# Performance work log

Hardware: AMD Instinct MI355X
Metric: run time of the kernel (lower is better)

Reference implementation:

```python
import jax, jax.numpy as jnp
import numpy as np

B = 32          # batch
NR = 1000       # n_reports
NP = 2000       # n_paths (candidate codes per lookup matrix)
NC = 3000       # n_codes (valid path / code entries)
NSNIP = 20000   # n_snippets
RV = 20000      # report word vocab
CV = 50000      # code word vocab
QL = 50         # report length (words)
S = 100         # num_snippet per code
L = 60          # len_snippet (words per snippet)
E = 300         # word embedding dim
DD = 100        # dim_dense
K = 5           # k_max_pool
NEG = 1.0e12


def setup_inputs() -> dict:
    key = jax.random.key(0)
    ks = jax.random.split(key, 16)
    f = jnp.float32
    sc = lambda n: 1.0 / float(np.sqrt(n))
    inp = {}
    inp["r_idx"] = jax.random.randint(ks[0], (B,), 0, NR)
    inp["c_idx"] = jax.random.randint(ks[1], (B,), 0, NP)
    # lookup tables stored as float (cast to int inside forward, as in torch)
    inp["matrix"] = jax.random.randint(ks[2], (NR, NP), 0, NC).astype(f)
    inp["report_table"] = jax.random.randint(ks[3], (NR, QL), 0, RV).astype(f)
    inp["report_word_emb"] = jax.random.normal(ks[4], (RV, E), dtype=f)
    inp["idf_table"] = jax.random.uniform(ks[5], (RV, 1), dtype=f, minval=0.5, maxval=6.0)
    inp["code_table"] = jax.random.randint(ks[6], (NC, S), 0, NSNIP).astype(f)
    inp["snippet_table"] = jax.random.randint(ks[7], (NSNIP, L), 0, CV).astype(f)
    inp["code_word_emb"] = jax.random.normal(ks[8], (CV, E), dtype=f)
    inp["snippet_len_table"] = jax.random.randint(ks[9], (NSNIP, 1), 1, L + 1).astype(f)
    inp["code_len_table"] = jax.random.randint(ks[10], (NP, 1), 1, S + 1).astype(f)
    # trainable relevance MLP + k-max fusion
    inp["W1"] = jax.random.uniform(ks[11], (E, DD), dtype=f, minval=-sc(E), maxval=sc(E))
    inp["b1"] = jnp.zeros((DD,), f)
    inp["W2"] = jax.random.uniform(ks[12], (DD, DD // 2), dtype=f, minval=-sc(DD), maxval=sc(DD))
    inp["b2"] = jnp.zeros((DD // 2,), f)
    inp["W3"] = jax.random.uniform(ks[13], (DD // 2, 1), dtype=f, minval=-sc(DD // 2), maxval=sc(DD // 2))
    inp["b3"] = jnp.zeros((1,), f)
    inp["Wk"] = jax.random.uniform(ks[14], (K, 1), dtype=f, minval=-sc(K), maxval=sc(K))
    inp["bk"] = jnp.zeros((1,), f)
    return inp


def _l2norm(x, axis):
    n = jnp.linalg.norm(x, ord=2, axis=axis, keepdims=True)
    y = x / n
    return jnp.where(jnp.isnan(y), 0.0, y)  # torch: NaN-fix after div


def reference(r_idx, c_idx, matrix, report_table, report_word_emb, idf_table,
              code_table, snippet_table, code_word_emb, snippet_len_table,
              code_len_table, W1, b1, W2, b2, W3, b3, Wk, bk):
    trans_c = matrix[r_idx, c_idx].astype(jnp.int32)            # (b,)
    r_vec = report_table[r_idx].astype(jnp.int32)               # (b,q)
    r_emb = report_word_emb[r_vec]                              # (b,q,e)
    c_snip = code_table[trans_c].astype(jnp.int32)              # (b,s)
    s_len = snippet_len_table[c_snip, 0].astype(jnp.int32)      # (b,s)
    c_words = snippet_table[c_snip].astype(jnp.int32)           # (b,s,l)
    c_emb = code_word_emb[c_words]                              # (b,s,l,e)
    s_mask = jnp.arange(L)[None, None, :] < s_len[:, :, None]   # (b,s,l)
    # masked dot attention: every report word attends within each snippet
    scores = jnp.einsum('bqe,bsle->bqsl', r_emb, c_emb)
    scores = scores - (~s_mask)[:, None, :, :].astype(scores.dtype) * NEG
    a = jax.nn.softmax(scores, axis=3)
    attn_v = jnp.einsum('bqsl,bsle->bqse', a, c_emb)            # (b,q,s,e)
    nc = _l2norm(attn_v, 3)                                     # (b,q,s,e)
    nr = _l2norm(r_emb, 2)                                      # (b,q,e)
    rc = nr[:, :, None, :] * nc                                 # (b,q,s,e)
    h = jnp.tanh(rc @ W1 + b1)
    h = jnp.tanh(h @ W2 + b2)
    rel = jnp.tanh(h @ W3 + b3)[..., 0]                         # (b,q,s)
    c_len = code_len_table[c_idx, 0].astype(jnp.int32)          # (b,)
    c_mask = (jnp.arange(S)[None, :] < c_len[:, None]).astype(rel.dtype)
    rel = rel * c_mask[:, None, :]
    topk = jax.lax.top_k(rel, K)[0]                             # (b,q,k)
    r_c = (topk @ Wk + bk)[..., 0]                              # (b,q)
    r_idf = idf_table[r_vec, 0]                                 # (b,q)
    r_idf = jnp.where(r_idf == 0.0, -NEG, r_idf)
    r_idf = jax.nn.softmax(r_idf, axis=1)
    return jnp.sum(r_c * r_idf, axis=1)                         # (b,)
```

## Files before the change

kernel.cpp:

```cpp
#include <hip/hip_runtime.h>
#include <math.h>

typedef __attribute__((ext_vector_type(8))) _Float16 half8;
typedef __attribute__((ext_vector_type(4))) _Float16 half4v;
typedef __attribute__((ext_vector_type(4))) float f32x4;

constexpr int cB = 32, cNP = 2000, cS = 100, cL = 60, cE = 300;
constexpr int cQ = 50, cDD = 100, cDH = 50;
constexpr float cNEG = 1.0e12f;

constexpr size_t OFF_REL  = 0;
constexpr size_t OFF_RG   = 160000;
constexpr size_t OFF_RNRM = 640000;
constexpr size_t OFF_IDFW = 641600;
constexpr size_t OFF_W1TH = 643200;
constexpr size_t OFF_W1TL = 660224;
constexpr size_t OFF_W2TH = 677248;
constexpr size_t OFF_W2TL = 681344;

constexpr int cH1S = 132;
constexpr int LDS_CL    = 0;
constexpr int LDS_AL    = 72000;
constexpr int LDS_AVF   = 84000;
constexpr int LDS_G_HI  = 0;
constexpr int LDS_G_LO  = 40960;
constexpr int LDS_H1    = 84000;
constexpr int LDS_H2    = 117792;
constexpr int LDS_SCL   = 144000;
constexpr int LDS_WORDS = 144256;
constexpr int LDS_TOTAL = 144512;

__device__ __forceinline__ _Float16 h_hi(float f) { return (_Float16)f; }
__device__ __forceinline__ _Float16 h_lo(float f, _Float16 h) { return (_Float16)(f - (float)h); }
__device__ __forceinline__ int bswz(int cb, int row) {
    return (cb & ~127) | ((cb & 127) ^ ((row & 7) << 4));
}

__global__ void prep_weights(const float* __restrict__ W1, const float* __restrict__ W2,
                             _Float16* __restrict__ W1TH, _Float16* __restrict__ W1TL,
                             _Float16* __restrict__ W2TH, _Float16* __restrict__ W2TL)
{
    int tid = blockIdx.x * blockDim.x + threadIdx.x;
    int stride = gridDim.x * blockDim.x;
    for (int idx = tid; idx < 112 * 304; idx += stride) {
        int d = idx / 304, e = idx % 304;
        float w = (d < cDD && e < cE) ? W1[(size_t)e * cDD + d] : 0.f;
        _Float16 h = h_hi(w);
        W1TH[idx] = h; W1TL[idx] = h_lo(w, h);
    }
    for (int idx = tid; idx < 64 * 128; idx += stride) {
        int j = idx / 128, d = idx % 128;
        float w = (j < cDH && d < cDD) ? W2[(size_t)d * cDH + j] : 0.f;
        _Float16 h = h_hi(w);
        W2TH[idx] = h; W2TL[idx] = h_lo(w, h);
    }
}

__global__ __launch_bounds__(256) void prep_batch(
    const int* __restrict__ r_idx,
    const float* __restrict__ report_table,
    const float* __restrict__ report_word_emb,
    const float* __restrict__ idf_table,
    float* __restrict__ Rg, float* __restrict__ rnorm, float* __restrict__ idfw)
{
    int b = blockIdx.x, tid = threadIdx.x;
    __shared__ int rv[cQ];
    if (tid < cQ) rv[tid] = (int)report_table[(size_t)r_idx[b] * cQ + tid];
    __syncthreads();
    float* dst = Rg + (size_t)b * cQ * cE;
    for (int idx = tid; idx < cQ * 75; idx += 256) {
        int q = idx / 75, e4 = idx % 75;
        f32x4 v = *(const f32x4*)(report_word_emb + (size_t)rv[q] * cE + e4 * 4);
        *(f32x4*)(dst + (size_t)q * cE + e4 * 4) = v;
    }
    __syncthreads();
    if (tid < cQ) {
        const float* row = dst + (size_t)tid * cE;
        float ss = 0.f;
        for (int e = 0; e < cE; e += 4) {
            f32x4 v = *(const f32x4*)(row + e);
            ss += v[0]*v[0] + v[1]*v[1] + v[2]*v[2] + v[3]*v[3];
        }
        rnorm[b * cQ + tid] = sqrtf(ss);
    }
    if (tid < 64) {
        float x = -INFINITY;
        if (tid < cQ) {
            float w = idf_table[rv[tid]];
            x = (w == 0.0f) ? -cNEG : w;
        }
        float m = x;
        for (int o = 32; o; o >>= 1) m = fmaxf(m, __shfl_xor(m, o));
        float e = (tid < cQ) ? expf(x - m) : 0.f;
        float ssum = e;
        for (int o = 32; o; o >>= 1) ssum += __shfl_xor(ssum, o);
        if (tid < cQ) idfw[b * cQ + tid] = e / ssum;
    }
}

__global__ __launch_bounds__(1024, 4) void kernelA(
    const int* __restrict__ r_idx, const int* __restrict__ c_idx,
    const float* __restrict__ matrix, const float* __restrict__ code_table,
    const float* __restrict__ snippet_table, const float* __restrict__ code_word_emb,
    const float* __restrict__ snippet_len_table,
    const float* __restrict__ Rg, const float* __restrict__ rnorm,
    const _Float16* __restrict__ W1TH, const _Float16* __restrict__ W1TL, const float* __restrict__ b1,
    const _Float16* __restrict__ W2TH, const _Float16* __restrict__ W2TL, const float* __restrict__ b2,
    const float* __restrict__ W3, const float* __restrict__ b3,
    float* __restrict__ rel_out)
{
    const int s = blockIdx.x, b = blockIdx.y;
    const int tid = threadIdx.x;
    const int lane = tid & 63, wid = tid >> 6;
    const int n = lane & 15, gl = lane >> 4;

    __shared__ __align__(16) unsigned char smem[LDS_TOTAL];
    int*   words = (int*)(smem + LDS_WORDS);
    float* sclp  = (float*)(smem + LDS_SCL);
    float* Cl    = (float*)(smem + LDS_CL);
    float* Alp   = (float*)(smem + LDS_AL);
    float* AVf   = (float*)(smem + LDS_AVF);
    float* Rlds  = (float*)(smem + LDS_AVF);

    const float* RgB = Rg + (size_t)b * cQ * cE;

    const int rr = r_idx[b], cc = c_idx[b];
    const int code = (int)matrix[(size_t)rr * cNP + cc];
    const int snip = (int)code_table[(size_t)code * cS + s];
    const int slen = (int)snippet_len_table[snip];

    if (tid < cL) words[tid] = (int)snippet_table[(size_t)snip * cL + tid];
    if (tid < cQ) sclp[tid] = 0.f;
    for (int idx = tid; idx < cQ * 75; idx += 1024) {
        int q = idx / 75, e4 = idx % 75;
        *(f32x4*)(Rlds + q * 300 + e4 * 4) = *(const f32x4*)(RgB + (size_t)q * cE + e4 * 4);
    }
    __syncthreads();

    for (int idx = tid; idx < cL * 75; idx += 1024) {
        int l = idx / 75, e4 = idx % 75;
        f32x4 v = *(const f32x4*)(code_word_emb + (size_t)words[l] * cE + e4 * 4);
        *(f32x4*)(Cl + l * 300 + e4 * 4) = v;
    }
    __syncthreads();

    {
        const int qt = tid >> 5, lt2 = tid & 31;
        float acc[2][2];
        #pragma unroll
        for (int i = 0; i < 2; i++)
            #pragma unroll
            for (int j = 0; j < 2; j++) acc[i][j] = 0.f;
        const float* rrow[2];
        #pragma unroll
        for (int i = 0; i < 2; i++) {
            int q = qt + 32 * i;
            rrow[i] = Rlds + (size_t)(q < cQ ? q : 0) * 300;
        }
        int lrow[2];
        #pragma unroll
        for (int j = 0; j < 2; j++) {
            int l = lt2 + 32 * j;
            lrow[j] = (l < cL) ? l : 0;
        }
        for (int e = 0; e < cE; e += 4) {
            f32x4 rv[2], cv[2];
            #pragma unroll
            for (int i = 0; i < 2; i++) rv[i] = *(const f32x4*)(rrow[i] + e);
            #pragma unroll
            for (int j = 0; j < 2; j++) cv[j] = *(const f32x4*)(Cl + lrow[j] * 300 + e);
            #pragma unroll
            for (int i = 0; i < 2; i++)
                #pragma unroll
                for (int j = 0; j < 2; j++)
                    acc[i][j] += rv[i][0] * cv[j][0] + rv[i][1] * cv[j][1] +
                                 rv[i][2] * cv[j][2] + rv[i][3] * cv[j][3];
        }
        #pragma unroll
        for (int i = 0; i < 2; i++) {
            int q = qt + 32 * i;
            if (q >= cQ) continue;
            #pragma unroll
            for (int j = 0; j < 2; j++) {
                int l = lt2 + 32 * j;
                if (l >= cL) continue;
                Alp[q * 60 + l] = acc[i][j] - ((l >= slen) ? cNEG : 0.f);
            }
        }
    }
    __syncthreads();

    {
        const int g2 = tid >> 2, k = tid & 3;
        if (g2 < cQ) {
            float v[15];
            float m = -INFINITY;
            #pragma unroll
            for (int t = 0; t < 15; t++) { v[t] = Alp[g2 * 60 + k + 4 * t]; m = fmaxf(m, v[t]); }
            m = fmaxf(m, __shfl_xor(m, 1));
            m = fmaxf(m, __shfl_xor(m, 2));
            float sum = 0.f;
            #pragma unroll
            for (int t = 0; t < 15; t++) { v[t] = expf(v[t] - m); sum += v[t]; }
            sum += __shfl_xor(sum, 1);
            sum += __shfl_xor(sum, 2);
            float inv = 1.0f / sum;
            #pragma unroll
            for (int t = 0; t < 15; t++) Alp[g2 * 60 + k + 4 * t] = v[t] * inv;
        }
    }
    __syncthreads();

    {
        const int qt3 = tid >> 5, et3 = tid & 31;
        const float* arow[2];
        int qv[2];
        #pragma unroll
        for (int i = 0; i < 2; i++) {
            int q = qt3 + 32 * i;
            qv[i] = q;
            arow[i] = Alp + (size_t)((q < cQ) ? q : 0) * 60;
        }
        int e4v[3], e4c[3];
        #pragma unroll
        for (int jj = 0; jj < 3; jj++) {
            e4v[jj] = et3 + 32 * jj;
            e4c[jj] = (e4v[jj] < 75) ? e4v[jj] : 0;
        }
        f32x4 acc4[2][3];
        #pragma unroll
        for (int i = 0; i < 2; i++)
            #pragma unroll
            for (int jj = 0; jj < 3; jj++) acc4[i][jj] = (f32x4){0.f, 0.f, 0.f, 0.f};
        for (int l = 0; l < cL; l++) {
            float av[2];
            #pragma unroll
            for (int i = 0; i < 2; i++) av[i] = arow[i][l];
            f32x4 cv[3];
            #pragma unroll
            for (int jj = 0; jj < 3; jj++) cv[jj] = *(const f32x4*)(Cl + l * 300 + e4c[jj] * 4);
            #pragma unroll
            for (int i = 0; i < 2; i++)
                #pragma unroll
                for (int jj = 0; jj < 3; jj++) {
                    acc4[i][jj][0] += av[i] * cv[jj][0];
                    acc4[i][jj][1] += av[i] * cv[jj][1];
                    acc4[i][jj][2] += av[i] * cv[jj][2];
                    acc4[i][jj][3] += av[i] * cv[jj][3];
                }
        }
        #pragma unroll
        for (int i = 0; i < 2; i++)
            #pragma unroll
            for (int jj = 0; jj < 3; jj++)
                if (e4v[jj] < 75 && qv[i] < cQ)
                    *(f32x4*)(AVf + qv[i] * 300 + e4v[jj] * 4) = acc4[i][jj];
    }
    __syncthreads();

    if (tid < 256) {
        const int qs = tid >> 4, es = tid & 15;
        #pragma unroll
        for (int jj = 0; jj < 5; jj++) {
            int e4 = es + 16 * jj;
            int e4cl = (e4 < 75) ? e4 : 0;
            #pragma unroll
            for (int i = 0; i < 4; i++) {
                int q = qs + 16 * i;
                int qcl = (q < cQ) ? q : 0;
                f32x4 v = *(const f32x4*)(AVf + qcl * 300 + e4cl * 4);
                bool valid = (e4 < 75) && (q < cQ);
                float dv = valid ? (v[0]*v[0] + v[1]*v[1] + v[2]*v[2] + v[3]*v[3]) : 0.f;
                dv += __shfl_xor(dv, 1);
                dv += __shfl_xor(dv, 2);
                dv += __shfl_xor(dv, 4);
                dv += __shfl_xor(dv, 8);
                if (es == 0 && q < cQ) sclp[q] += dv;
            }
        }
    }
    __syncthreads();

    if (tid < cQ) {
        float p = rnorm[b * cQ + tid] * sqrtf(sclp[tid]);
        sclp[tid] = (p > 0.f) ? (1.0f / p) : 0.f;
    }

    {
        for (int idx = tid; idx < 64 * 80; idx += 1024) {
            int q = idx / 80, e4 = idx % 80;
            half4v h4 = {0, 0, 0, 0}, l4 = {0, 0, 0, 0};
            if (q < cQ && e4 < 75) {
                f32x4 av4 = *(const f32x4*)(AVf + q * 300 + e4 * 4);
                f32x4 rv4 = *(const f32x4*)(RgB + (size_t)q * cE + e4 * 4);
                #pragma unroll
                for (int k = 0; k < 4; k++) {
                    float gf = av4[k] * rv4[k];
                    h4[k] = h_hi(gf);
                    l4[k] = h_lo(gf, h4[k]);
                }
            }
            int bo = q * 640 + bswz(8 * e4, q);
            *(half4v*)(smem + LDS_G_HI + bo) = h4;
            *(half4v*)(smem + LDS_G_LO + bo) = l4;
        }
    }
    __syncthreads();

    {
        const half8 z8 = {0,0,0,0,0,0,0,0};
        const int dt = wid & 7;
        const int q2b = (wid >> 3) * 2;
        f32x4 accH[2];
        #pragma unroll
        for (int t = 0; t < 2; t++) accH[t] = (f32x4){0.f, 0.f, 0.f, 0.f};
        if (dt < 7) {
            #pragma unroll
            for (int ks = 0; ks < 10; ks++) {
                bool lv = (ks != 9) || (gl < 2);
                half8 gh[2], glo[2];
                #pragma unroll
                for (int t = 0; t < 2; t++) {
                    gh[t] = z8; glo[t] = z8;
                    if (lv) {
                        int q = 16 * (q2b + t) + n;
                        int bo = q * 640 + bswz(64 * ks + 16 * gl, q);
                        gh[t]  = *(const half8*)(smem + LDS_G_HI + bo);
                        glo[t] = *(const half8*)(smem + LDS_G_LO + bo);
                    }
                }
                half8 wh = z8, wl = z8;
                if (lv) {
                    int d = 16 * dt + n;
                    wh = *(const half8*)(W1TH + (size_t)d * 304 + 32 * ks + 8 * gl);
                    wl = *(const half8*)(W1TL + (size_t)d * 304 + 32 * ks + 8 * gl);
                }
                #pragma unroll
                for (int t = 0; t < 2; t++) {
                    accH[t] = __builtin_amdgcn_mfma_f32_16x16x32_f16(gh[t],  wh, accH[t], 0, 0, 0);
                    accH[t] = __builtin_amdgcn_mfma_f32_16x16x32_f16(gh[t],  wl, accH[t], 0, 0, 0);
                    accH[t] = __builtin_amdgcn_mfma_f32_16x16x32_f16(glo[t], wh, accH[t], 0, 0, 0);
                }
            }
        }
        float* h1p = (float*)(smem + LDS_H1);
        if (dt < 7) {
            int d = 16 * dt + n;
            #pragma unroll
            for (int t = 0; t < 2; t++)
                #pragma unroll
                for (int r = 0; r < 4; r++) {
                    int q = 16 * (q2b + t) + 4 * gl + r;
                    if (q < cQ) {
                        float v = (d < cDD) ? tanhf(accH[t][r] * sclp[q] + b1[d]) : 0.f;
                        h1p[q * cH1S + d] = v;
                    }
                }
        }
        for (int idx = tid; idx < cQ * 16; idx += 1024) {
            int q = idx >> 4, d = 112 + (idx & 15);
            h1p[q * cH1S + d] = 0.f;
        }
    }
    __syncthreads();

    {
        const float* h1p = (const float*)(smem + LDS_H1);
        const int jw = 16 * (wid & 3) + n;
        const int q2 = wid >> 2;
        f32x4 accJ = (f32x4){0.f, 0.f, 0.f, 0.f};
        #pragma unroll
        for (int ks = 0; ks < 4; ks++) {
            int q = 16 * q2 + n;
            const float* p = h1p + q * cH1S + 32 * ks + 8 * gl;
            f32x4 fa = *(const f32x4*)p;
            f32x4 fb = *(const f32x4*)(p + 4);
            half8 h8, l8;
            #pragma unroll
            for (int jj = 0; jj < 8; jj++) {
                float f = (jj < 4) ? fa[jj] : fb[jj - 4];
                _Float16 h = h_hi(f);
                h8[jj] = h;
                l8[jj] = h_lo(f, h);
            }
            half8 wh = *(const half8*)(W2TH + (size_t)jw * 128 + 32 * ks + 8 * gl);
            half8 wl = *(const half8*)(W2TL + (size_t)jw * 128 + 32 * ks + 8 * gl);
            accJ = __builtin_amdgcn_mfma_f32_16x16x32_f16(h8, wh, accJ, 0, 0, 0);
            accJ = __builtin_amdgcn_mfma_f32_16x16x32_f16(h8, wl, accJ, 0, 0, 0);
            accJ = __builtin_amdgcn_mfma_f32_16x16x32_f16(l8, wh, accJ, 0, 0, 0);
        }
        float* h2p = (float*)(smem + LDS_H2);
        #pragma unroll
        for (int r = 0; r < 4; r++) {
            int q = 16 * q2 + 4 * gl + r;
            if (q < cQ && jw < cDH) h2p[q * 68 + jw] = tanhf(accJ[r] + b2[jw]);
        }
    }
    __syncthreads();

    if (tid < cQ) {
        const float* h2p = (const float*)(smem + LDS_H2);
        float a = b3[0];
        #pragma unroll 10
        for (int jj = 0; jj < cDH; jj++) a += h2p[tid * 68 + jj] * W3[jj];
        rel_out[((size_t)b * cQ + tid) * cS + s] = tanhf(a);
    }
}

__global__ __launch_bounds__(64) void kernelB(
    const float* __restrict__ rel_ws, const float* __restrict__ idfw,
    const int* __restrict__ c_idx, const float* __restrict__ code_len_table,
    const float* __restrict__ Wk, const float* __restrict__ bk,
    float* __restrict__ out)
{
    int b = blockIdx.x, q = threadIdx.x;
    float val = 0.f;
    if (q < cQ) {
        int clen = (int)code_len_table[c_idx[b]];
        const float* row = rel_ws + ((size_t)b * cQ + q) * cS;
        float t0 = -INFINITY, t1 = -INFINITY, t2 = -INFINITY, t3 = -INFINITY, t4 = -INFINITY;
        for (int s = 0; s < cS; s++) {
            float v = row[s] * ((s < clen) ? 1.f : 0.f);
            float m0 = fmaxf(t0, v), n0 = fminf(t0, v);
            float m1 = fmaxf(t1, n0), n1 = fminf(t1, n0);
            float m2 = fmaxf(t2, n1), n2 = fminf(t2, n1);
            float m3 = fmaxf(t3, n2), n3 = fminf(t3, n2);
            float m4 = fmaxf(t4, n3);
            t0 = m0; t1 = m1; t2 = m2; t3 = m3; t4 = m4;
        }
        float rc = t0 * Wk[0] + t1 * Wk[1] + t2 * Wk[2] + t3 * Wk[3] + t4 * Wk[4] + bk[0];
        val = rc * idfw[b * cQ + q];
    }
    for (int o = 32; o; o >>= 1) val += __shfl_down(val, o);
    if (q == 0) out[b] = val;
}

extern "C" void kernel_launch(void* const* d_in, const int* in_sizes, int n_in,
                              void* d_out, int out_size, void* d_ws, size_t ws_size,
                              hipStream_t stream)
{
    const int*   r_idx             = (const int*)d_in[0];
    const int*   c_idx             = (const int*)d_in[1];
    const float* matrix            = (const float*)d_in[2];
    const float* report_table      = (const float*)d_in[3];
    const float* report_word_emb   = (const float*)d_in[4];
    const float* idf_table         = (const float*)d_in[5];
    const float* code_table        = (const float*)d_in[6];
    const float* snippet_table     = (const float*)d_in[7];
    const float* code_word_emb     = (const float*)d_in[8];
    const float* snippet_len_table = (const float*)d_in[9];
    const float* code_len_table    = (const float*)d_in[10];
    const float* W1 = (const float*)d_in[11];
    const float* b1 = (const float*)d_in[12];
    const float* W2 = (const float*)d_in[13];
    const float* b2 = (const float*)d_in[14];
    const float* W3 = (const float*)d_in[15];
    const float* b3 = (const float*)d_in[16];
    const float* Wk = (const float*)d_in[17];
    const float* bk = (const float*)d_in[18];
    float* out = (float*)d_out;
    float* ws  = (float*)d_ws;

    float* rel_ws = ws + OFF_REL;
    float* Rg     = ws + OFF_RG;
    float* rnormp = ws + OFF_RNRM;
    float* idfwp  = ws + OFF_IDFW;
    _Float16* W1THp = (_Float16*)(ws + OFF_W1TH);
    _Float16* W1TLp = (_Float16*)(ws + OFF_W1TL);
    _Float16* W2THp = (_Float16*)(ws + OFF_W2TH);
    _Float16* W2TLp = (_Float16*)(ws + OFF_W2TL);

    prep_weights<<<64, 256, 0, stream>>>(W1, W2, W1THp, W1TLp, W2THp, W2TLp);
    prep_batch<<<cB, 256, 0, stream>>>(r_idx, report_table, report_word_emb, idf_table,
                                       Rg, rnormp, idfwp);
    kernelA<<<dim3(cS, cB), 1024, 0, stream>>>(r_idx, c_idx, matrix, code_table,
                                               snippet_table, code_word_emb, snippet_len_table,
                                               Rg, rnormp,
                                               W1THp, W1TLp, b1, W2THp, W2TLp, b2, W3, b3, rel_ws);
    kernelB<<<cB, 64, 0, stream>>>(rel_ws, idfwp, c_idx, code_len_table, Wk, bk, out);
}
```

Baseline: 558.5 us.

## Shrink LDS footprint by reading embeddings from global and packing fp16 splits on the fly

Drops the LDS staging of the report and code embeddings, so the score and attention-value loops read them straight from global memory (cache). The fp16 hi/lo split buffers are no longer stored in LDS; the split is done in registers right before each MFMA, and the h1 buffer stride shrinks. Together this cuts LDS use from about 141 KB to about 79 KB, which is meant to let two 1024-thread blocks share a CU, and the launch-bounds hint is raised to match. The cost is more global/L2 traffic, with each block re-reading rows from cache, and repeated conversion work in the MLP loop.

```diff
diff --git a/kernel.cpp b/kernel.cpp
--- a/kernel.cpp
+++ b/kernel.cpp
@@ -2,7 +2,6 @@
 #include <math.h>
 
 typedef __attribute__((ext_vector_type(8))) _Float16 half8;
-typedef __attribute__((ext_vector_type(4))) _Float16 half4v;
 typedef __attribute__((ext_vector_type(4))) float f32x4;
 
 constexpr int cB = 32, cNP = 2000, cS = 100, cL = 60, cE = 300;
@@ -18,23 +17,17 @@
 constexpr size_t OFF_W2TH = 677248;
 constexpr size_t OFF_W2TL = 681344;
 
-constexpr int cH1S = 132;
-constexpr int LDS_CL    = 0;
-constexpr int LDS_AL    = 72000;
-constexpr int LDS_AVF   = 84000;
-constexpr int LDS_G_HI  = 0;
-constexpr int LDS_G_LO  = 40960;
-constexpr int LDS_H1    = 84000;
-constexpr int LDS_H2    = 117792;
-constexpr int LDS_SCL   = 144000;
-constexpr int LDS_WORDS = 144256;
-constexpr int LDS_TOTAL = 144512;
+constexpr int LDS_AV    = 0;
+constexpr int LDS_AL    = 60000;
+constexpr int LDS_H1    = 60000;
+constexpr int LDS_H1Z   = 80000;
+constexpr int LDS_H2    = 0;
+constexpr int LDS_SCL   = 80128;
+constexpr int LDS_WORDS = 80384;
+constexpr int LDS_TOTAL = 80640;
 
 __device__ __forceinline__ _Float16 h_hi(float f) { return (_Float16)f; }
 __device__ __forceinline__ _Float16 h_lo(float f, _Float16 h) { return (_Float16)(f - (float)h); }
-__device__ __forceinline__ int bswz(int cb, int row) {
-    return (cb & ~127) | ((cb & 127) ^ ((row & 7) << 4));
-}
 
 __global__ void prep_weights(const float* __restrict__ W1, const float* __restrict__ W2,
                              _Float16* __restrict__ W1TH, _Float16* __restrict__ W1TL,
@@ -98,7 +91,7 @@
     }
 }
 
-__global__ __launch_bounds__(1024, 4) void kernelA(
+__global__ __launch_bounds__(1024, 8) void kernelA(
     const int* __restrict__ r_idx, const int* __restrict__ c_idx,
     const float* __restrict__ matrix, const float* __restrict__ code_table,
     const float* __restrict__ snippet_table, const float* __restrict__ code_word_emb,
@@ -117,10 +110,8 @@
     __shared__ __align__(16) unsigned char smem[LDS_TOTAL];
     int*   words = (int*)(smem + LDS_WORDS);
     float* sclp  = (float*)(smem + LDS_SCL);
-    float* Cl    = (float*)(smem + LDS_CL);
     float* Alp   = (float*)(smem + LDS_AL);
-    float* AVf   = (float*)(smem + LDS_AVF);
-    float* Rlds  = (float*)(smem + LDS_AVF);
+    float* AVf   = (float*)(smem + LDS_AV);
 
     const float* RgB = Rg + (size_t)b * cQ * cE;
 
@@ -131,17 +122,6 @@
 
     if (tid < cL) words[tid] = (int)snippet_table[(size_t)snip * cL + tid];
     if (tid < cQ) sclp[tid] = 0.f;
-    for (int idx = tid; idx < cQ * 75; idx += 1024) {
-        int q = idx / 75, e4 = idx % 75;
-        *(f32x4*)(Rlds + q * 300 + e4 * 4) = *(const f32x4*)(RgB + (size_t)q * cE + e4 * 4);
-    }
-    __syncthreads();
-
-    for (int idx = tid; idx < cL * 75; idx += 1024) {
-        int l = idx / 75, e4 = idx % 75;
-        f32x4 v = *(const f32x4*)(code_word_emb + (size_t)words[l] * cE + e4 * 4);
-        *(f32x4*)(Cl + l * 300 + e4 * 4) = v;
-    }
     __syncthreads();
 
     {
@@ -155,20 +135,20 @@
         #pragma unroll
         for (int i = 0; i < 2; i++) {
             int q = qt + 32 * i;
-            rrow[i] = Rlds + (size_t)(q < cQ ? q : 0) * 300;
-        }
-        int lrow[2];
+            rrow[i] = RgB + (size_t)(q < cQ ? q : 0) * cE;
+        }
+        const float* crow[2];
         #pragma unroll
         for (int j = 0; j < 2; j++) {
             int l = lt2 + 32 * j;
-            lrow[j] = (l < cL) ? l : 0;
+            crow[j] = code_word_emb + (size_t)words[(l < cL) ? l : 0] * cE;
         }
         for (int e = 0; e < cE; e += 4) {
             f32x4 rv[2], cv[2];
             #pragma unroll
             for (int i = 0; i < 2; i++) rv[i] = *(const f32x4*)(rrow[i] + e);
             #pragma unroll
-            for (int j = 0; j < 2; j++) cv[j] = *(const f32x4*)(Cl + lrow[j] * 300 + e);
+            for (int j = 0; j < 2; j++) cv[j] = *(const f32x4*)(crow[j] + e);
             #pragma unroll
             for (int i = 0; i < 2; i++)
                 #pragma unroll
@@ -236,9 +216,10 @@
             float av[2];
             #pragma unroll
             for (int i = 0; i < 2; i++) av[i] = arow[i][l];
+            const float* crl = code_word_emb + (size_t)words[l] * cE;
             f32x4 cv[3];
             #pragma unroll
-            for (int jj = 0; jj < 3; jj++) cv[jj] = *(const f32x4*)(Cl + l * 300 + e4c[jj] * 4);
+            for (int jj = 0; jj < 3; jj++) cv[jj] = *(const f32x4*)(crl + e4c[jj] * 4);
             #pragma unroll
             for (int i = 0; i < 2; i++)
                 #pragma unroll
@@ -285,25 +266,14 @@
         float p = rnorm[b * cQ + tid] * sqrtf(sclp[tid]);
         sclp[tid] = (p > 0.f) ? (1.0f / p) : 0.f;
     }
-
-    {
-        for (int idx = tid; idx < 64 * 80; idx += 1024) {
-            int q = idx / 80, e4 = idx % 80;
-            half4v h4 = {0, 0, 0, 0}, l4 = {0, 0, 0, 0};
-            if (q < cQ && e4 < 75) {
-                f32x4 av4 = *(const f32x4*)(AVf + q * 300 + e4 * 4);
-                f32x4 rv4 = *(const f32x4*)(RgB + (size_t)q * cE + e4 * 4);
-                #pragma unroll
-                for (int k = 0; k < 4; k++) {
-                    float gf = av4[k] * rv4[k];
-                    h4[k] = h_hi(gf);
-                    l4[k] = h_lo(gf, h4[k]);
-                }
-            }
-            int bo = q * 640 + bswz(8 * e4, q);
-            *(half4v*)(smem + LDS_G_HI + bo) = h4;
-            *(half4v*)(smem + LDS_G_LO + bo) = l4;
-        }
+    for (int idx = tid; idx < cQ * 75; idx += 1024) {
+        int q = idx / 75, e4 = idx % 75;
+        f32x4 av4 = *(const f32x4*)(AVf + q * 300 + e4 * 4);
+        f32x4 rv4 = *(const f32x4*)(RgB + (size_t)q * cE + e4 * 4);
+        f32x4 g4;
+        #pragma unroll
+        for (int k = 0; k < 4; k++) g4[k] = av4[k] * rv4[k];
+        *(f32x4*)(AVf + q * 300 + e4 * 4) = g4;
     }
     __syncthreads();
 
@@ -322,11 +292,19 @@
                 #pragma unroll
                 for (int t = 0; t < 2; t++) {
                     gh[t] = z8; glo[t] = z8;
-                    if (lv) {
-                        int q = 16 * (q2b + t) + n;
-                        int bo = q * 640 + bswz(64 * ks + 16 * gl, q);
-                        gh[t]  = *(const half8*)(smem + LDS_G_HI + bo);
-                        glo[t] = *(const half8*)(smem + LDS_G_LO + bo);
+                    int q = 16 * (q2b + t) + n;
+                    if (lv && q < cQ) {
+                        const float* gp = AVf + q * 300 + 32 * ks + 8 * gl;
+                        f32x4 fa = *(const f32x4*)gp;
+                        f32x4 fb = (ks == 9 && gl == 1) ? (f32x4){0.f,0.f,0.f,0.f}
+                                                        : *(const f32x4*)(gp + 4);
+                        #pragma unroll
+                        for (int k = 0; k < 8; k++) {
+                            float f = (k < 4) ? fa[k] : fb[k - 4];
+                            _Float16 h = h_hi(f);
+                            gh[t][k]  = h;
+                            glo[t][k] = h_lo(f, h);
+                        }
                     }
                 }
                 half8 wh = z8, wl = z8;
@@ -351,37 +329,35 @@
                 #pragma unroll
                 for (int r = 0; r < 4; r++) {
                     int q = 16 * (q2b + t) + 4 * gl + r;
-                    if (q < cQ) {
-                        float v = (d < cDD) ? tanhf(accH[t][r] * sclp[q] + b1[d]) : 0.f;
-                        h1p[q * cH1S + d] = v;
-                    }
-                }
-        }
-        for (int idx = tid; idx < cQ * 16; idx += 1024) {
-            int q = idx >> 4, d = 112 + (idx & 15);
-            h1p[q * cH1S + d] = 0.f;
-        }
+                    if (q < cQ && d < cDD)
+                        h1p[q * 100 + d] = tanhf(accH[t][r] * sclp[q] + b1[d]);
+                }
+        }
+        if (tid < 32) ((float*)(smem + LDS_H1Z))[tid] = 0.f;
     }
     __syncthreads();
 
     {
         const float* h1p = (const float*)(smem + LDS_H1);
+        const half8 z8 = {0,0,0,0,0,0,0,0};
         const int jw = 16 * (wid & 3) + n;
         const int q2 = wid >> 2;
         f32x4 accJ = (f32x4){0.f, 0.f, 0.f, 0.f};
         #pragma unroll
         for (int ks = 0; ks < 4; ks++) {
             int q = 16 * q2 + n;
-            const float* p = h1p + q * cH1S + 32 * ks + 8 * gl;
-            f32x4 fa = *(const f32x4*)p;
-            f32x4 fb = *(const f32x4*)(p + 4);
-            half8 h8, l8;
-            #pragma unroll
-            for (int jj = 0; jj < 8; jj++) {
-                float f = (jj < 4) ? fa[jj] : fb[jj - 4];
-                _Float16 h = h_hi(f);
-                h8[jj] = h;
-                l8[jj] = h_lo(f, h);
+            half8 h8 = z8, l8 = z8;
+            if (q < cQ) {
+                const float* p = h1p + q * 100 + 32 * ks + 8 * gl;
+                f32x4 fa = *(const f32x4*)p;
+                f32x4 fb = *(const f32x4*)(p + 4);
+                #pragma unroll
+                for (int jj = 0; jj < 8; jj++) {
+                    float f = (jj < 4) ? fa[jj] : fb[jj - 4];
+                    _Float16 h = h_hi(f);
+                    h8[jj] = h;
+                    l8[jj] = h_lo(f, h);
+                }
             }
             half8 wh = *(const half8*)(W2TH + (size_t)jw * 128 + 32 * ks + 8 * gl);
             half8 wl = *(const half8*)(W2TL + (size_t)jw * 128 + 32 * ks + 8 * gl);
@@ -389,6 +365,7 @@
             accJ = __builtin_amdgcn_mfma_f32_16x16x32_f16(h8, wl, accJ, 0, 0, 0);
             accJ = __builtin_amdgcn_mfma_f32_16x16x32_f16(l8, wh, accJ, 0, 0, 0);
         }
+        __syncthreads();
         float* h2p = (float*)(smem + LDS_H2);
         #pragma unroll
         for (int r = 0; r < 4; r++) {
```

Result: slower. 1.225 ms (+119.4%).
